# Optimization experiments

Hardware: AMD Instinct MI355X
Metric: run time of the kernel (lower is better)

The kernel has to match this reference:

```python
import jax, jax.numpy as jnp
import numpy as np

N, T = 128, 20
E_IN, E_EMB, E_RNN = 2, 64, 256
N_IN, N_EMB, N_RNN, N_OUT = 2, 64, 128, 5
ATT = 64

# static edge index sets: diagonal = temporal edges (i,i), off-diagonal = spatial edges (i,j)
_DIAG = np.arange(N) * N + np.arange(N)
_OFFJ = np.array([[j for j in range(N) if j != i] for i in range(N)])  # [N, N-1]
_OFFD = (np.arange(N)[:, None] * N + _OFFJ).reshape(-1)               # [N*(N-1)]
_TEMP = (N - 1) / np.sqrt(ATT)  # attention temperature = num_edges / sqrt(attention_size)


def setup_inputs() -> dict:
    ks = iter(jax.random.split(jax.random.key(0), 40))
    def p(shape, s=0.05):
        return jax.random.normal(next(ks), shape, jnp.float32) * s
    return {
        "nodes": p((T, N, N_IN), 1.0),
        "edges": p((T, N * N, E_IN), 1.0),
        "h_edge0": jnp.zeros((N * N, E_RNN), jnp.float32),
        "c_edge0": jnp.zeros((N * N, E_RNN), jnp.float32),
        "h_node0": jnp.zeros((N, N_RNN), jnp.float32),
        "c_node0": jnp.zeros((N, N_RNN), jnp.float32),
        "t_enc_w": p((E_EMB, E_IN)), "t_enc_b": p((E_EMB,)),
        "t_wih": p((4 * E_RNN, E_EMB)), "t_whh": p((4 * E_RNN, E_RNN)),
        "t_bih": p((4 * E_RNN,)), "t_bhh": p((4 * E_RNN,)),
        "s_enc_w": p((E_EMB, E_IN)), "s_enc_b": p((E_EMB,)),
        "s_wih": p((4 * E_RNN, E_EMB)), "s_whh": p((4 * E_RNN, E_RNN)),
        "s_bih": p((4 * E_RNN,)), "s_bhh": p((4 * E_RNN,)),
        "att_t_w": p((ATT, E_RNN)), "att_t_b": p((ATT,)),
        "att_s_w": p((ATT, E_RNN)), "att_s_b": p((ATT,)),
        "n_enc_w": p((N_EMB, N_IN)), "n_enc_b": p((N_EMB,)),
        "n_attn_w": p((N_EMB, 2 * E_RNN)), "n_attn_b": p((N_EMB,)),
        "n_wih": p((4 * N_RNN, 2 * N_EMB)), "n_whh": p((4 * N_RNN, N_RNN)),
        "n_bih": p((4 * N_RNN,)), "n_bhh": p((4 * N_RNN,)),
        "out_w": p((N_OUT, N_RNN)), "out_b": p((N_OUT,)),
    }


def _lstm(x, h, c, wih, whh, bih, bhh):
    g = x @ wih.T + bih + h @ whh.T + bhh
    i, f, gg, o = jnp.split(g, 4, axis=-1)
    c2 = jax.nn.sigmoid(f) * c + jax.nn.sigmoid(i) * jnp.tanh(gg)
    return jax.nn.sigmoid(o) * jnp.tanh(c2), c2


def reference(nodes, edges, h_edge0, c_edge0, h_node0, c_node0,
              t_enc_w, t_enc_b, t_wih, t_whh, t_bih, t_bhh,
              s_enc_w, s_enc_b, s_wih, s_whh, s_bih, s_bhh,
              att_t_w, att_t_b, att_s_w, att_s_b,
              n_enc_w, n_enc_b, n_attn_w, n_attn_b,
              n_wih, n_whh, n_bih, n_bhh, out_w, out_b):
    def step(carry, xt):
        h_e, c_e, h_n, c_n = carry
        pos_t, edg_t = xt
        # temporal edge RNN on self edges (i,i)
        x_t = jax.nn.relu(edg_t[_DIAG] @ t_enc_w.T + t_enc_b)
        h_t, c_t = _lstm(x_t, h_e[_DIAG], c_e[_DIAG], t_wih, t_whh, t_bih, t_bhh)
        # spatial edge RNN on all pairwise edges (i,j), i != j
        x_s = jax.nn.relu(edg_t[_OFFD] @ s_enc_w.T + s_enc_b)
        h_s, c_s = _lstm(x_s, h_e[_OFFD], c_e[_OFFD], s_wih, s_whh, s_bih, s_bhh)
        h_e = h_e.at[_DIAG].set(h_t).at[_OFFD].set(h_s)
        c_e = c_e.at[_DIAG].set(c_t).at[_OFFD].set(c_s)
        # attention: each node attends over its N-1 spatial edge hidden states
        hs = h_s.reshape(N, N - 1, E_RNN)
        te = h_t @ att_t_w.T + att_t_b                          # [N, ATT]
        se = jnp.einsum('nkd,ad->nka', hs, att_s_w) + att_s_b   # [N, N-1, ATT]
        logits = jnp.einsum('nka,na->nk', se, te) * _TEMP
        w = jax.nn.softmax(logits, axis=-1)
        weighted = jnp.einsum('nk,nkd->nd', w, hs)              # [N, E_RNN]
        # node RNN
        enc = jax.nn.relu(pos_t @ n_enc_w.T + n_enc_b)
        h_edges = jnp.concatenate([h_t, weighted], axis=-1)
        h_emb = jax.nn.relu(h_edges @ n_attn_w.T + n_attn_b)
        h_n, c_n = _lstm(jnp.concatenate([enc, h_emb], axis=-1), h_n, c_n,
                         n_wih, n_whh, n_bih, n_bhh)
        out = h_n @ out_w.T + out_b
        return (h_e, c_e, h_n, c_n), out

    _, outs = jax.lax.scan(step, (h_edge0, c_edge0, h_node0, c_node0), (nodes, edges))
    return outs  # [T, N, 5]
```

## Files before the change

kernel.cpp:

```cpp
#include <hip/hip_runtime.h>
#include <cmath>

#define NN 128
#define TT 20
#define ERNN 256
#define TEMPSC 15.875f

typedef __attribute__((ext_vector_type(8))) short bf16x8;
typedef __attribute__((ext_vector_type(4))) float f32x4;

__device__ __forceinline__ float sigm(float x){ return 1.f/(1.f+__expf(-x)); }
__device__ __forceinline__ float ftanh(float x){ float e = __expf(2.f*x); return 1.f - 2.f/(e + 1.f); }
__device__ __forceinline__ float b2f(unsigned short u){ union{unsigned int i; float f;} v; v.i = ((unsigned int)u)<<16; return v.f; }
__device__ __forceinline__ unsigned short f2b(float x){ union{float f; unsigned int u;} v; v.f = x; unsigned int r = v.u + 0x7fffu + ((v.u>>16)&1u); return (unsigned short)(r>>16); }

typedef __attribute__((address_space(3))) unsigned int lds_u32;
typedef __attribute__((address_space(1))) unsigned int glb_u32;
__device__ __forceinline__ void glds16(const void* g, void* l){
    __builtin_amdgcn_global_load_lds((const glb_u32*)g, (lds_u32*)l, 16, 0, 0);
}

__device__ __forceinline__ size_t hoff(int r, int d){
    return ((size_t)((r>>7)*32 + (d>>3))*128 + (r&127))*8 + (d&7);
}

#define R_W2    (2*1024*320)
#define R_EB    2048
#define R_NWT   131072
#define R_NBS   512
#define R_HNN   16384
#define R_CNN   16384
#define R_INIT  (16384*32)
#define R_XENC  ((size_t)TT*16384*8)
#define PREP_TOT (R_W2 + R_EB + R_NWT + R_NBS + R_HNN + R_CNN + R_INIT + R_XENC)

__global__ void k_prep_all(
    const float* __restrict__ s_wih, const float* __restrict__ s_whh, unsigned short* __restrict__ s_wHi,
    const float* __restrict__ t_wih, const float* __restrict__ t_whh, unsigned short* __restrict__ t_wHi,
    const float* __restrict__ s_bih, const float* __restrict__ s_bhh, float* __restrict__ s_bs,
    const float* __restrict__ t_bih, const float* __restrict__ t_bhh, float* __restrict__ t_bs,
    const float* __restrict__ n_wih, const float* __restrict__ n_whh, float* __restrict__ n_wT,
    const float* __restrict__ n_bih, const float* __restrict__ n_bhh, float* __restrict__ n_bs,
    const float* __restrict__ h_n0, float* __restrict__ h_nn,
    const float* __restrict__ c_n0, float* __restrict__ c_nn,
    const float* __restrict__ h_e0, const float* __restrict__ c_e0,
    unsigned short* __restrict__ hHi, unsigned short* __restrict__ c_b,
    const float* __restrict__ edges,
    const float* __restrict__ s_enc_w, const float* __restrict__ s_enc_b,
    const float* __restrict__ t_enc_w, const float* __restrict__ t_enc_b,
    unsigned short* __restrict__ xe)
{
    size_t i = (size_t)blockIdx.x*256 + threadIdx.x;
    if (i < R_W2) {
        int idx = (int)i;
        int which = idx >= 1024*320;
        if (which) idx -= 1024*320;
        const float* wih = which ? t_wih : s_wih;
        const float* whh = which ? t_whh : s_whh;
        unsigned short* wHi = which ? t_wHi : s_wHi;
        int c = idx / 320, k = idx - c*320;
        int ch = ((c>>6)<<4) + (c&15), g = (c>>4)&3;
        int r = g*256 + ch;
        float v = (k < 64) ? wih[r*64 + k] : whh[r*256 + (k-64)];
        size_t dst = ((size_t)((c>>7)*40 + (k>>3))*128 + (c&127))*8 + (k&7);
        wHi[dst] = f2b(v);
        return;
    }
    i -= R_W2;
    if (i < R_EB) {
        int c = (int)i, which = c >= 1024;
        if (which) c -= 1024;
        const float* bih = which ? t_bih : s_bih;
        const float* bhh = which ? t_bhh : s_bhh;
        float* bs = which ? t_bs : s_bs;
        int ch = ((c>>6)<<4)+(c&15), g=(c>>4)&3;
        int r = g*256+ch;
        bs[c] = bih[r] + bhh[r];
        return;
    }
    i -= R_EB;
    if (i < R_NWT) {
        int j = (int)i;
        if (j < 65536) { int r = j >> 7, c = j & 127; n_wT[c*512 + r] = n_wih[j]; }
        else { j -= 65536; int r = j >> 7, c = j & 127; n_wT[(128 + c)*512 + r] = n_whh[j]; }
        return;
    }
    i -= R_NWT;
    if (i < R_NBS) { n_bs[i] = n_bih[i] + n_bhh[i]; return; }
    i -= R_NBS;
    if (i < R_HNN) { h_nn[i] = h_n0[i]; return; }
    i -= R_HNN;
    if (i < R_CNN) { c_nn[i] = c_n0[i]; return; }
    i -= R_CNN;
    if (i < R_INIT) {
        int g = (int)i;
        int d8 = g & 31, r = g >> 5;
        int row_ij;
        if (r < 16256){ int ii = r/127, jj = r - ii*127; row_ij = ii*NN + jj + (jj>=ii ? 1:0); }
        else          { row_ij = (r - 16256)*(NN+1); }
        const float* hs = h_e0 + (size_t)row_ij*ERNN + d8*8;
        const float* cs = c_e0 + (size_t)row_ij*ERNN + d8*8;
        bf16x8 hb, cb;
        #pragma unroll
        for (int q = 0; q < 8; ++q){ hb[q] = (short)f2b(hs[q]); cb[q] = (short)f2b(cs[q]); }
        *(bf16x8*)&hHi[hoff(r, d8*8)] = hb;
        *(bf16x8*)&c_b[(size_t)r*ERNN + d8*8] = cb;
        return;
    }
    i -= R_INIT;
    if (i < R_XENC) {
        size_t g = i;
        int row = (int)(g & 127);
        size_t rest = g >> 7;
        int kc = (int)(rest & 7);
        int tile = (int)((rest >> 3) & 127);
        int t = (int)(rest >> 10);
        int r = tile*128 + row;
        bool sp = (r < 16256);
        int row_ij;
        if (sp) { int ii = r/127, jj = r - ii*127; row_ij = ii*NN + jj + (jj>=ii ? 1:0); }
        else    { row_ij = (r - 16256)*(NN+1); }
        const float* w = sp ? s_enc_w : t_enc_w;
        const float* b = sp ? s_enc_b : t_enc_b;
        float e0 = edges[((size_t)t*16384 + row_ij)*2];
        float e1 = edges[((size_t)t*16384 + row_ij)*2 + 1];
        bf16x8 v8;
        #pragma unroll
        for (int q = 0; q < 8; ++q) {
            int m = kc*8 + q;
            v8[q] = (short)f2b(fmaxf(fmaf(w[m*2], e0, fmaf(w[m*2+1], e1, b[m])), 0.f));
        }
        *(bf16x8*)&xe[g*8] = v8;
    }
}

#define ESTEP(KS, NW) do { \
    asm volatile("s_waitcnt vmcnt(" #NW ")" ::: "memory"); \
    __builtin_amdgcn_s_barrier(); \
    __builtin_amdgcn_sched_barrier(0); \
    bf16x8 a0 = *(const bf16x8*)&Ah[(KS)&1][(kg*128 + arow)*8]; \
    bf16x8 a1 = *(const bf16x8*)&Ah[(KS)&1][(kg*128 + arow + 16)*8]; \
    bf16x8 b0 = *(const bf16x8*)&Bh[(KS)&1][(kg*128 + bcol)*8]; \
    bf16x8 b1 = *(const bf16x8*)&Bh[(KS)&1][(kg*128 + bcol + 16)*8]; \
    bf16x8 b2 = *(const bf16x8*)&Bh[(KS)&1][(kg*128 + bcol + 32)*8]; \
    bf16x8 b3 = *(const bf16x8*)&Bh[(KS)&1][(kg*128 + bcol + 48)*8]; \
    asm volatile("s_waitcnt lgkmcnt(0)" ::: "memory"); \
    __builtin_amdgcn_sched_barrier(0); \
    __builtin_amdgcn_s_barrier(); \
    if ((KS) + 2 <= 9) stage((KS)+2, (KS)&1); \
    acc[0][0] = __builtin_amdgcn_mfma_f32_16x16x32_bf16(a0, b0, acc[0][0],0,0,0); \
    acc[0][1] = __builtin_amdgcn_mfma_f32_16x16x32_bf16(a0, b1, acc[0][1],0,0,0); \
    acc[0][2] = __builtin_amdgcn_mfma_f32_16x16x32_bf16(a0, b2, acc[0][2],0,0,0); \
    acc[0][3] = __builtin_amdgcn_mfma_f32_16x16x32_bf16(a0, b3, acc[0][3],0,0,0); \
    acc[1][0] = __builtin_amdgcn_mfma_f32_16x16x32_bf16(a1, b0, acc[1][0],0,0,0); \
    acc[1][1] = __builtin_amdgcn_mfma_f32_16x16x32_bf16(a1, b1, acc[1][1],0,0,0); \
    acc[1][2] = __builtin_amdgcn_mfma_f32_16x16x32_bf16(a1, b2, acc[1][2],0,0,0); \
    acc[1][3] = __builtin_amdgcn_mfma_f32_16x16x32_bf16(a1, b3, acc[1][3],0,0,0); \
} while(0)

__global__ __launch_bounds__(512) void k_fused(
    const unsigned short* __restrict__ xenc_t,
    const unsigned short* __restrict__ h_in, unsigned short* __restrict__ h_out,
    unsigned short* __restrict__ hl_out, unsigned short* __restrict__ c_b,
    const unsigned short* __restrict__ s_wHi, const float* __restrict__ s_bs,
    const unsigned short* __restrict__ t_wHi, const float* __restrict__ t_bs,
    int has_node, int n_edge,
    const float* __restrict__ nodes_prev, const unsigned short* __restrict__ hl_prev,
    float* __restrict__ h_nn, float* __restrict__ c_nn, float* __restrict__ out_prev,
    const float* __restrict__ att_t_w, const float* __restrict__ att_t_b,
    const float* __restrict__ att_s_w, const float* __restrict__ att_s_b,
    const float* __restrict__ n_enc_w, const float* __restrict__ n_enc_b,
    const float* __restrict__ n_attn_w, const float* __restrict__ n_attn_b,
    const float* __restrict__ n_wT, const float* __restrict__ n_bsum,
    const float* __restrict__ out_w, const float* __restrict__ out_b)
{
    __shared__ __align__(16) char smem[32768];
    const int bid = blockIdx.x, tid = threadIdx.x;

    if (bid < NN) {
        if (!has_node) return;
        const int i = bid;
        float* sm  = (float*)smem;
        float* ht  = sm;
        float* te  = sm + 256;
        float* u   = sm + 320;
        float* lg  = sm + 576;
        float* cat = sm + 704;
        float* xc  = sm + 1216;
        float* hnl = sm + 1344;
        float* gl  = sm + 1472;
        float* pws = sm + 1984;
        float* msc = sm + 4032;

        if (tid < 256) ht[tid] = b2f(hl_prev[(size_t)(16256 + i)*256 + tid]);
        __syncthreads();
        if (tid < 256) {
            int m = tid >> 2, q = tid & 3;
            float s = 0.f;
            const float* wr = att_t_w + m*ERNN + q*64;
            const float* hh = ht + q*64;
            #pragma unroll 8
            for (int k = 0; k < 64; ++k) s = fmaf(wr[k], hh[k], s);
            s += __shfl_xor(s, 1);
            s += __shfl_xor(s, 2);
            if (q == 0) te[m] = s + att_t_b[m];
        }
        __syncthreads();
        if (tid < 256) {
            float s = 0.f;
            for (int m = 0; m < 64; ++m) s = fmaf(att_s_w[m*ERNN + tid], te[m], s);
            u[tid] = s;
        }
        if (tid == 320) {
            float s = 0.f;
            for (int m = 0; m < 64; ++m) s = fmaf(te[m], att_s_b[m], s);
            msc[2] = s;
        }
        __syncthreads();
        {
            int slot = tid >> 2, q = tid & 3;
            float part = 0.f;
            if (slot < 127) {
                const unsigned short* hs = hl_prev + (size_t)(i*127 + slot)*256 + q*64;
                const float* uu = u + q*64;
                #pragma unroll
                for (int d8 = 0; d8 < 8; ++d8) {
                    bf16x8 v = *(const bf16x8*)(hs + d8*8);
                    #pragma unroll
                    for (int j = 0; j < 8; ++j)
                        part = fmaf(uu[d8*8 + j], b2f((unsigned short)v[j]), part);
                }
            }
            part += __shfl_xor(part, 1);
            part += __shfl_xor(part, 2);
            if (slot < 127 && q == 0) lg[slot] = (part + msc[2]) * TEMPSC;
            if (tid == 511) lg[127] = -1e30f;
        }
        __syncthreads();
        if (tid < 64) {
            float a = fmaxf(lg[tid], lg[tid+64]);
            for (int off = 32; off; off >>= 1) a = fmaxf(a, __shfl_xor(a, off));
            if (tid == 0) msc[0] = a;
        }
        __syncthreads();
        if (tid < 128) lg[tid] = (tid < 127) ? __expf(lg[tid] - msc[0]) : 0.f;
        __syncthreads();
        if (tid < 64) {
            float a = lg[tid] + lg[tid+64];
            for (int off = 32; off; off >>= 1) a += __shfl_xor(a, off);
            if (tid == 0) msc[1] = a;
        }
        __syncthreads();
        {
            int w = tid >> 6, lane = tid & 63;
            float a0 = 0.f, a1 = 0.f, a2 = 0.f, a3 = 0.f;
            #pragma unroll 4
            for (int s = w*16; s < w*16 + 16; ++s) {
                int srow = (s < 127) ? s : 0;
                float wgt = lg[s];
                const unsigned short* hs = hl_prev + (size_t)(i*127 + srow)*256 + lane*4;
                ushort4 v = *(const ushort4*)hs;
                a0 = fmaf(wgt, b2f(v.x), a0);
                a1 = fmaf(wgt, b2f(v.y), a1);
                a2 = fmaf(wgt, b2f(v.z), a2);
                a3 = fmaf(wgt, b2f(v.w), a3);
            }
            pws[w*256 + lane*4+0] = a0; pws[w*256 + lane*4+1] = a1;
            pws[w*256 + lane*4+2] = a2; pws[w*256 + lane*4+3] = a3;
        }
        if (tid >= 256 && tid < 384) hnl[tid-256] = h_nn[i*128 + (tid-256)];
        __syncthreads();
        if (tid < 256) {
            float s = 0.f;
            #pragma unroll
            for (int w = 0; w < 8; ++w) s += pws[w*256 + tid];
            cat[256 + tid] = s / msc[1];
            cat[tid] = ht[tid];
        }
        __syncthreads();
        if (tid < 64) {
            float p0 = nodes_prev[i*2], p1 = nodes_prev[i*2+1];
            xc[tid] = fmaxf(fmaf(n_enc_w[tid*2], p0, fmaf(n_enc_w[tid*2+1], p1, n_enc_b[tid])), 0.f);
        }
        if (tid >= 256) {
            int t2 = tid - 256;
            int m = t2 >> 2, q = t2 & 3;
            float s = 0.f;
            const float* wr = n_attn_w + m*512 + q*128;
            const float* cc = cat + q*128;
            #pragma unroll 8
            for (int d = 0; d < 128; ++d) s = fmaf(wr[d], cc[d], s);
            s += __shfl_xor(s, 1);
            s += __shfl_xor(s, 2);
            if (q == 0) xc[64 + m] = fmaxf(s + n_attn_b[m], 0.f);
        }
        __syncthreads();
        {
            int n = tid;
            float s = n_bsum[n];
            for (int k = 0; k < 128; ++k) s = fmaf(n_wT[k*512 + n], xc[k], s);
            for (int k = 0; k < 128; ++k) s = fmaf(n_wT[(128+k)*512 + n], hnl[k], s);
            gl[n] = s;
        }
        __syncthreads();
        if (tid < 128) {
            float co = c_nn[i*128 + tid];
            float c2 = sigm(gl[128+tid])*co + sigm(gl[tid])*ftanh(gl[256+tid]);
            float h2 = sigm(gl[384+tid])*ftanh(c2);
            c_nn[i*128+tid] = c2;
            h_nn[i*128+tid] = h2;
            hnl[tid] = h2;
        }
        __syncthreads();
        if (tid < 5) {
            float s = out_b[tid];
            const float* wr = out_w + tid*128;
            for (int k = 0; k < 128; ++k) s = fmaf(wr[k], hnl[k], s);
            out_prev[i*5 + tid] = s;
        }
        return;
    }

    if (!n_edge) return;
    unsigned short (*Ah)[4096] = (unsigned short(*)[4096])smem;
    unsigned short (*Bh)[4096] = (unsigned short(*)[4096])(smem + 16384);
    const int ebid = bid - NN;
    const int lane = tid & 63, wid = tid >> 6;
    const int wg = (ebid & 7)*128 + (ebid >> 3);
    const int bm = wg >> 3, ntp = wg & 7;
    const bool sp = (bm < 127);
    const int rbase = bm * 128;
    const unsigned short* wHi = sp ? s_wHi : t_wHi;
    const float* bs = sp ? s_bs : t_bs;
    const int wr = wid & 3, wc = wid >> 2;
    const int nt = ntp*2 + wc;

    auto stage = [&](int ks, int b){
        int kc = wid >> 1, half = wid & 1;
        const unsigned short* asrc = (ks < 2)
            ? xenc_t + ((size_t)bm*8  + ks*4     + kc)*1024 + half*512
            : h_in   + ((size_t)bm*32 + (ks-2)*4 + kc)*1024 + half*512;
        glds16(asrc + lane*8, (char*)&Ah[b][0] + wid*1024);
        size_t wb = ((size_t)(ntp*40 + ks*4 + kc)*128 + half*64)*8;
        glds16(wHi + wb + lane*8, (char*)&Bh[b][0] + wid*1024);
    };
    stage(0, 0);
    stage(1, 1);

    f32x4 acc[2][4];
    #pragma unroll
    for (int m = 0; m < 2; ++m)
        #pragma unroll
        for (int g = 0; g < 4; ++g)
            acc[m][g] = (f32x4){0.f,0.f,0.f,0.f};

    const int arow = wr*32 + (lane & 15);
    const int bcol = wc*64 + (lane & 15);
    const int kg = lane >> 4;

    ESTEP(0, 2);
    ESTEP(1, 2);
    ESTEP(2, 2);
    ESTEP(3, 2);
    ESTEP(4, 2);
    ESTEP(5, 2);
    ESTEP(6, 2);
    ESTEP(7, 2);
    ESTEP(8, 2);
    ESTEP(9, 0);

    const int chl = lane & 15, q4 = (lane >> 4)*4;
    const int ch = nt*16 + chl;
    const int cbase = nt*64 + chl;
    const float b0 = bs[cbase], b1 = bs[cbase+16], b2 = bs[cbase+32], b3 = bs[cbase+48];
    #pragma unroll
    for (int m = 0; m < 2; ++m) {
        #pragma unroll
        for (int rg = 0; rg < 4; ++rg) {
            int lrow = wr*32 + m*16 + q4 + rg;
            int row = rbase + lrow;
            float gi = acc[m][0][rg] + b0;
            float gf = acc[m][1][rg] + b1;
            float gg = acc[m][2][rg] + b2;
            float go = acc[m][3][rg] + b3;
            size_t off = (size_t)row*256 + ch;
            float c_old = b2f(c_b[off]);
            float c2 = sigm(gf)*c_old + sigm(gi)*ftanh(gg);
            float h2 = sigm(go)*ftanh(c2);
            c_b[off] = f2b(c2);
            unsigned short hb = f2b(h2);
            h_out[((size_t)(bm*32 + (ch>>3))*128 + lrow)*8 + (ch&7)] = hb;
            hl_out[off] = hb;
        }
    }
}

extern "C" void kernel_launch(void* const* d_in, const int* in_sizes, int n_in,
                              void* d_out, int out_size, void* d_ws, size_t ws_size,
                              hipStream_t stream)
{
    const float* nodes   = (const float*)d_in[0];
    const float* edges   = (const float*)d_in[1];
    const float* h_e0    = (const float*)d_in[2];
    const float* c_e0    = (const float*)d_in[3];
    const float* h_n0    = (const float*)d_in[4];
    const float* c_n0    = (const float*)d_in[5];
    const float* t_enc_w = (const float*)d_in[6];
    const float* t_enc_b = (const float*)d_in[7];
    const float* t_wih   = (const float*)d_in[8];
    const float* t_whh   = (const float*)d_in[9];
    const float* t_bih   = (const float*)d_in[10];
    const float* t_bhh   = (const float*)d_in[11];
    const float* s_enc_w = (const float*)d_in[12];
    const float* s_enc_b = (const float*)d_in[13];
    const float* s_wih   = (const float*)d_in[14];
    const float* s_whh   = (const float*)d_in[15];
    const float* s_bih   = (const float*)d_in[16];
    const float* s_bhh   = (const float*)d_in[17];
    const float* att_t_w = (const float*)d_in[18];
    const float* att_t_b = (const float*)d_in[19];
    const float* att_s_w = (const float*)d_in[20];
    const float* att_s_b = (const float*)d_in[21];
    const float* n_enc_w = (const float*)d_in[22];
    const float* n_enc_b = (const float*)d_in[23];
    const float* n_attn_w= (const float*)d_in[24];
    const float* n_attn_b= (const float*)d_in[25];
    const float* n_wih   = (const float*)d_in[26];
    const float* n_whh   = (const float*)d_in[27];
    const float* n_bih   = (const float*)d_in[28];
    const float* n_bhh   = (const float*)d_in[29];
    const float* out_w   = (const float*)d_in[30];
    const float* out_b   = (const float*)d_in[31];
    float* out = (float*)d_out;

    char* p = (char*)d_ws;
    float* h_nn  = (float*)p;            p += 128*128*4;
    float* c_nn  = (float*)p;            p += 128*128*4;
    float* s_bs  = (float*)p;            p += 1024*4;
    float* t_bs  = (float*)p;            p += 1024*4;
    float* n_wT  = (float*)p;            p += 256*512*4;
    float* n_bs  = (float*)p;            p += 512*4;
    unsigned short* c_b  = (unsigned short*)p;  p += (size_t)16384*256*2;
    unsigned short* h_a  = (unsigned short*)p;  p += (size_t)16384*256*2;
    unsigned short* h_b  = (unsigned short*)p;  p += (size_t)16384*256*2;
    unsigned short* hl_a = (unsigned short*)p;  p += (size_t)16384*256*2;
    unsigned short* hl_b = (unsigned short*)p;  p += (size_t)16384*256*2;
    unsigned short* xenc = (unsigned short*)p;  p += (size_t)TT*16384*64*2;
    unsigned short* s_wHi = (unsigned short*)p; p += 1024*320*2;
    unsigned short* t_wHi = (unsigned short*)p; p += 1024*320*2;

    int prep_blocks = (int)((PREP_TOT + 255) / 256);
    k_prep_all<<<prep_blocks, 256, 0, stream>>>(
        s_wih, s_whh, s_wHi, t_wih, t_whh, t_wHi,
        s_bih, s_bhh, s_bs, t_bih, t_bhh, t_bs,
        n_wih, n_whh, n_wT, n_bih, n_bhh, n_bs,
        h_n0, h_nn, c_n0, c_nn,
        h_e0, c_e0, h_a, c_b,
        edges, s_enc_w, s_enc_b, t_enc_w, t_enc_b, xenc);

    for (int t = 0; t < TT; ++t) {
        const unsigned short* h_in  = (t & 1) ? h_b : h_a;
        unsigned short*       h_out = (t & 1) ? h_a : h_b;
        unsigned short*       hl_out= (t & 1) ? hl_b : hl_a;
        const unsigned short* hl_prev=(t & 1) ? hl_a : hl_b;
        const float* nprev = (t > 0) ? nodes + (size_t)(t-1)*NN*2 : nodes;
        float* oprev = (t > 0) ? out + (size_t)(t-1)*NN*5 : out;
        k_fused<<<NN + 1024, 512, 0, stream>>>(xenc + (size_t)t*16384*64,
            h_in, h_out, hl_out, c_b,
            s_wHi, s_bs, t_wHi, t_bs,
            (t > 0) ? 1 : 0, 1024,
            nprev, hl_prev, h_nn, c_nn, oprev,
            att_t_w, att_t_b, att_s_w, att_s_b, n_enc_w, n_enc_b,
            n_attn_w, n_attn_b, n_wT, n_bs, out_w, out_b);
    }
    k_fused<<<NN, 512, 0, stream>>>(xenc,
        h_a, h_b, hl_a, c_b,
        s_wHi, s_bs, t_wHi, t_bs,
        1, 0,
        nodes + (size_t)19*NN*2, hl_b, h_nn, c_nn, out + (size_t)19*NN*5,
        att_t_w, att_t_b, att_s_w, att_s_b, n_enc_w, n_enc_b,
        n_attn_w, n_attn_b, n_wT, n_bs, out_w, out_b);
}
```

Before: 609.5 us.

## Compute edge encoder on the fly into LDS inside fused LSTM kernel

Removes the precomputed bf16 edge-encoding buffer built in the prep kernel. Each GEMM block now computes relu(enc_w·edge+enc_b) for its 128 rows directly into the first two A-tile LDS buffers, and only streams the weight B tiles for those k-steps. This cuts the prep kernel's large write and the per-step global reads of the encoded tensor. In exchange it adds ALU work and small scattered edge loads at the start of every block, and the wait counts in the first step are changed to match.

```diff
diff --git a/kernel.cpp b/kernel.cpp
--- a/kernel.cpp
+++ b/kernel.cpp
@@ -31,8 +31,7 @@
 #define R_HNN   16384
 #define R_CNN   16384
 #define R_INIT  (16384*32)
-#define R_XENC  ((size_t)TT*16384*8)
-#define PREP_TOT (R_W2 + R_EB + R_NWT + R_NBS + R_HNN + R_CNN + R_INIT + R_XENC)
+#define PREP_TOT (R_W2 + R_EB + R_NWT + R_NBS + R_HNN + R_CNN + R_INIT)
 
 __global__ void k_prep_all(
     const float* __restrict__ s_wih, const float* __restrict__ s_whh, unsigned short* __restrict__ s_wHi,
@@ -44,11 +43,7 @@
     const float* __restrict__ h_n0, float* __restrict__ h_nn,
     const float* __restrict__ c_n0, float* __restrict__ c_nn,
     const float* __restrict__ h_e0, const float* __restrict__ c_e0,
-    unsigned short* __restrict__ hHi, unsigned short* __restrict__ c_b,
-    const float* __restrict__ edges,
-    const float* __restrict__ s_enc_w, const float* __restrict__ s_enc_b,
-    const float* __restrict__ t_enc_w, const float* __restrict__ t_enc_b,
-    unsigned short* __restrict__ xe)
+    unsigned short* __restrict__ hHi, unsigned short* __restrict__ c_b)
 {
     size_t i = (size_t)blockIdx.x*256 + threadIdx.x;
     if (i < R_W2) {
@@ -106,31 +101,6 @@
         *(bf16x8*)&hHi[hoff(r, d8*8)] = hb;
         *(bf16x8*)&c_b[(size_t)r*ERNN + d8*8] = cb;
         return;
-    }
-    i -= R_INIT;
-    if (i < R_XENC) {
-        size_t g = i;
-        int row = (int)(g & 127);
-        size_t rest = g >> 7;
-        int kc = (int)(rest & 7);
-        int tile = (int)((rest >> 3) & 127);
-        int t = (int)(rest >> 10);
-        int r = tile*128 + row;
-        bool sp = (r < 16256);
-        int row_ij;
-        if (sp) { int ii = r/127, jj = r - ii*127; row_ij = ii*NN + jj + (jj>=ii ? 1:0); }
-        else    { row_ij = (r - 16256)*(NN+1); }
-        const float* w = sp ? s_enc_w : t_enc_w;
-        const float* b = sp ? s_enc_b : t_enc_b;
-        float e0 = edges[((size_t)t*16384 + row_ij)*2];
-        float e1 = edges[((size_t)t*16384 + row_ij)*2 + 1];
-        bf16x8 v8;
-        #pragma unroll
-        for (int q = 0; q < 8; ++q) {
-            int m = kc*8 + q;
-            v8[q] = (short)f2b(fmaxf(fmaf(w[m*2], e0, fmaf(w[m*2+1], e1, b[m])), 0.f));
-        }
-        *(bf16x8*)&xe[g*8] = v8;
     }
 }
 
@@ -159,11 +129,13 @@
 } while(0)
 
 __global__ __launch_bounds__(512) void k_fused(
-    const unsigned short* __restrict__ xenc_t,
+    const float* __restrict__ edges_t,
     const unsigned short* __restrict__ h_in, unsigned short* __restrict__ h_out,
     unsigned short* __restrict__ hl_out, unsigned short* __restrict__ c_b,
     const unsigned short* __restrict__ s_wHi, const float* __restrict__ s_bs,
     const unsigned short* __restrict__ t_wHi, const float* __restrict__ t_bs,
+    const float* __restrict__ s_enc_w, const float* __restrict__ s_enc_b,
+    const float* __restrict__ t_enc_w, const float* __restrict__ t_enc_b,
     int has_node, int n_edge,
     const float* __restrict__ nodes_prev, const unsigned short* __restrict__ hl_prev,
     float* __restrict__ h_nn, float* __restrict__ c_nn, float* __restrict__ out_prev,
@@ -181,16 +153,11 @@
         if (!has_node) return;
         const int i = bid;
         float* sm  = (float*)smem;
-        float* ht  = sm;
-        float* te  = sm + 256;
-        float* u   = sm + 320;
-        float* lg  = sm + 576;
-        float* cat = sm + 704;
-        float* xc  = sm + 1216;
-        float* hnl = sm + 1344;
-        float* gl  = sm + 1472;
-        float* pws = sm + 1984;
-        float* msc = sm + 4032;
+        float* ht  = sm;           float* te  = sm + 256;
+        float* u   = sm + 320;     float* lg  = sm + 576;
+        float* cat = sm + 704;     float* xc  = sm + 1216;
+        float* hnl = sm + 1344;    float* gl  = sm + 1472;
+        float* pws = sm + 1984;    float* msc = sm + 4032;
 
         if (tid < 256) ht[tid] = b2f(hl_prev[(size_t)(16256 + i)*256 + tid]);
         __syncthreads();
@@ -332,20 +299,46 @@
     const int rbase = bm * 128;
     const unsigned short* wHi = sp ? s_wHi : t_wHi;
     const float* bs = sp ? s_bs : t_bs;
+    const float* enc_w = sp ? s_enc_w : t_enc_w;
+    const float* enc_b = sp ? s_enc_b : t_enc_b;
     const int wr = wid & 3, wc = wid >> 2;
     const int nt = ntp*2 + wc;
 
+    auto stageB = [&](int ks, int b){
+        int kc = wid >> 1, half = wid & 1;
+        size_t wb = ((size_t)(ntp*40 + ks*4 + kc)*128 + half*64)*8;
+        glds16(wHi + wb + lane*8, (char*)&Bh[b][0] + wid*1024);
+    };
     auto stage = [&](int ks, int b){
         int kc = wid >> 1, half = wid & 1;
-        const unsigned short* asrc = (ks < 2)
-            ? xenc_t + ((size_t)bm*8  + ks*4     + kc)*1024 + half*512
-            : h_in   + ((size_t)bm*32 + (ks-2)*4 + kc)*1024 + half*512;
+        const unsigned short* asrc =
+            h_in + ((size_t)bm*32 + (ks-2)*4 + kc)*1024 + half*512;
         glds16(asrc + lane*8, (char*)&Ah[b][0] + wid*1024);
         size_t wb = ((size_t)(ntp*40 + ks*4 + kc)*128 + half*64)*8;
         glds16(wHi + wb + lane*8, (char*)&Bh[b][0] + wid*1024);
     };
-    stage(0, 0);
-    stage(1, 1);
+
+    stageB(0, 0);
+    stageB(1, 1);
+
+    #pragma unroll
+    for (int rep = 0; rep < 2; ++rep) {
+        int c = rep*512 + tid;
+        int row = c & 127, kcg = c >> 7;
+        int r = rbase + row;
+        int row_ij;
+        if (sp) { int ii = r/127, jj = r - ii*127; row_ij = ii*NN + jj + (jj>=ii ? 1:0); }
+        else    { row_ij = (r - 16256)*(NN+1); }
+        float e0 = edges_t[row_ij*2], e1 = edges_t[row_ij*2+1];
+        bf16x8 ph;
+        #pragma unroll
+        for (int q = 0; q < 8; ++q) {
+            int m = kcg*8 + q;
+            ph[q] = (short)f2b(fmaxf(fmaf(enc_w[m*2], e0, fmaf(enc_w[m*2+1], e1, enc_b[m])), 0.f));
+        }
+        *(bf16x8*)&Ah[kcg>>2][((kcg&3)*128 + row)*8] = ph;
+    }
+    asm volatile("s_waitcnt lgkmcnt(0)" ::: "memory");
 
     f32x4 acc[2][4];
     #pragma unroll
@@ -358,7 +351,7 @@
     const int bcol = wc*64 + (lane & 15);
     const int kg = lane >> 4;
 
-    ESTEP(0, 2);
+    ESTEP(0, 1);
     ESTEP(1, 2);
     ESTEP(2, 2);
     ESTEP(3, 2);
@@ -445,7 +438,6 @@
     unsigned short* h_b  = (unsigned short*)p;  p += (size_t)16384*256*2;
     unsigned short* hl_a = (unsigned short*)p;  p += (size_t)16384*256*2;
     unsigned short* hl_b = (unsigned short*)p;  p += (size_t)16384*256*2;
-    unsigned short* xenc = (unsigned short*)p;  p += (size_t)TT*16384*64*2;
     unsigned short* s_wHi = (unsigned short*)p; p += 1024*320*2;
     unsigned short* t_wHi = (unsigned short*)p; p += 1024*320*2;
 
@@ -455,8 +447,7 @@
         s_bih, s_bhh, s_bs, t_bih, t_bhh, t_bs,
         n_wih, n_whh, n_wT, n_bih, n_bhh, n_bs,
         h_n0, h_nn, c_n0, c_nn,
-        h_e0, c_e0, h_a, c_b,
-        edges, s_enc_w, s_enc_b, t_enc_w, t_enc_b, xenc);
+        h_e0, c_e0, h_a, c_b);
 
     for (int t = 0; t < TT; ++t) {
         const unsigned short* h_in  = (t & 1) ? h_b : h_a;
@@ -465,17 +456,19 @@
         const unsigned short* hl_prev=(t & 1) ? hl_a : hl_b;
         const float* nprev = (t > 0) ? nodes + (size_t)(t-1)*NN*2 : nodes;
         float* oprev = (t > 0) ? out + (size_t)(t-1)*NN*5 : out;
-        k_fused<<<NN + 1024, 512, 0, stream>>>(xenc + (size_t)t*16384*64,
+        k_fused<<<NN + 1024, 512, 0, stream>>>(edges + (size_t)t*16384*2,
             h_in, h_out, hl_out, c_b,
             s_wHi, s_bs, t_wHi, t_bs,
+            s_enc_w, s_enc_b, t_enc_w, t_enc_b,
             (t > 0) ? 1 : 0, 1024,
             nprev, hl_prev, h_nn, c_nn, oprev,
             att_t_w, att_t_b, att_s_w, att_s_b, n_enc_w, n_enc_b,
             n_attn_w, n_attn_b, n_wT, n_bs, out_w, out_b);
     }
-    k_fused<<<NN, 512, 0, stream>>>(xenc,
+    k_fused<<<NN, 512, 0, stream>>>(edges,
         h_a, h_b, hl_a, c_b,
         s_wHi, s_bs, t_wHi, t_bs,
+        s_enc_w, s_enc_b, t_enc_w, t_enc_b,
         1, 0,
         nodes + (size_t)19*NN*2, hl_b, h_nn, c_nn, out + (size_t)19*NN*5,
         att_t_w, att_t_b, att_s_w, att_s_b, n_enc_w, n_enc_b,
```

After: 666.6 us. 9.4% more time.
